# Optimization experiments

Measured on AMD Instinct MI355X. Metric: run time of the kernel, lower is better.

Reference implementation:

```python
import jax, jax.numpy as jnp
import numpy as np

EPS = 1e-12  # matches torch F.normalize default eps

def setup_inputs() -> dict:
    key = jax.random.key(0)
    k1, k2 = jax.random.split(key)
    n, d = 8192, 1024
    x = jax.random.normal(k1, (n, d), dtype=jnp.float32)
    weight = jax.random.normal(k2, (d, d), dtype=jnp.float32) * (2.0 / d) ** 0.5
    return {"x": x, "weight": weight}

def reference(x, weight):
    # L2-normalize rows (torch F.normalize, dim=1): x / max(||x||_2, eps)
    nrm = jnp.sqrt(jnp.sum(x * x, axis=1, keepdims=True))
    norm = x / jnp.maximum(nrm, EPS)
    # adjacency: cosine-similarity Gram matrix [n, n] (materialized as in source)
    adj = norm @ norm.T
    ax = adj @ x          # [n, d]
    axw = ax @ weight     # [n, d]
    return axw
```

## Files before the change

### kernel.cpp

```cpp
#include <hip/hip_runtime.h>
#include <stdint.h>

typedef unsigned short u16;
typedef unsigned int u32;
typedef __attribute__((ext_vector_type(8))) short short8;
typedef __attribute__((ext_vector_type(4))) float floatx4;

__device__ __forceinline__ u16 f2b(float f) {
    u32 u = __builtin_bit_cast(u32, f);
    return (u16)((u + 0x7fffu + ((u >> 16) & 1u)) >> 16);
}

__device__ __forceinline__ void gld16(const void* g, void* l) {
    __builtin_amdgcn_global_load_lds(
        (const __attribute__((address_space(1))) u32*)g,
        (__attribute__((address_space(3))) u32*)l, 16, 0, 0);
}

__global__ __launch_bounds__(256) void fuse_prep(
    const float* __restrict__ x, u16* __restrict__ YT, u16* __restrict__ Yn) {
    __shared__ float tile[32][129];
    int r0 = blockIdx.x * 32;
    int t = threadIdx.x;
    int tg = t >> 5, tl = t & 31;
    float ss[4] = {0.f, 0.f, 0.f, 0.f};
    for (int c = 0; c < 8; c++) {
        #pragma unroll
        for (int i = 0; i < 4; i++) {
            int rr = i * 8 + tg;
            float4 v = *(const float4*)(x + (long)(r0 + rr) * 1024 + c * 128 + tl * 4);
            ss[i] += v.x * v.x + v.y * v.y + v.z * v.z + v.w * v.w;
        }
    }
    float rs_[4], sr_[4];
    #pragma unroll
    for (int i = 0; i < 4; i++) {
        #pragma unroll
        for (int m = 16; m > 0; m >>= 1) ss[i] += __shfl_xor(ss[i], m);
        float rcp = 1.0f / fmaxf(sqrtf(ss[i]), 1e-12f);
        rs_[i] = rcp;
        sr_[i] = sqrtf(rcp);
    }
    for (int c = 0; c < 8; c++) {
        __syncthreads();
        #pragma unroll
        for (int i = 0; i < 4; i++) {
            int rr = i * 8 + tg;
            float4 v = *(const float4*)(x + (long)(r0 + rr) * 1024 + c * 128 + tl * 4);
            ushort4 o;
            o.x = f2b(v.x * rs_[i]); o.y = f2b(v.y * rs_[i]);
            o.z = f2b(v.z * rs_[i]); o.w = f2b(v.w * rs_[i]);
            *(ushort4*)(Yn + (long)(r0 + rr) * 1024 + c * 128 + tl * 4) = o;
            tile[rr][tl * 4 + 0] = v.x * sr_[i];
            tile[rr][tl * 4 + 1] = v.y * sr_[i];
            tile[rr][tl * 4 + 2] = v.z * sr_[i];
            tile[rr][tl * 4 + 3] = v.w * sr_[i];
        }
        __syncthreads();
        #pragma unroll
        for (int i = 0; i < 4; i++) {
            int lin = i * 256 + t;
            int cc = lin >> 3, r4 = (lin & 7) << 2;
            ushort4 o;
            o.x = f2b(tile[r4 + 0][cc]); o.y = f2b(tile[r4 + 1][cc]);
            o.z = f2b(tile[r4 + 2][cc]); o.w = f2b(tile[r4 + 3][cc]);
            *(ushort4*)(YT + (long)(c * 128 + cc) * 8192 + r0 + r4) = o;
        }
    }
}

__global__ __launch_bounds__(256) void transpose_scale_dual(
    const float* __restrict__ src, const float* __restrict__ sr,
    u16* __restrict__ dstT, u16* __restrict__ dstR, int rows, int cols) {
    __shared__ float tile[64][65];
    __shared__ float rbuf[64];
    int r0 = blockIdx.x * 64, c0 = blockIdx.y * 64;
    int t = threadIdx.x;
    if (t < 64) rbuf[t] = (sr != nullptr) ? sr[r0 + t] : 1.0f;
    __syncthreads();
    #pragma unroll
    for (int i = 0; i < 4; i++) {
        int lin = i * 256 + t;
        int rr = lin >> 4, c4 = (lin & 15) << 2;
        float4 v = *(const float4*)(src + (long)(r0 + rr) * cols + c0 + c4);
        float s = rbuf[rr];
        v.x *= s; v.y *= s; v.z *= s; v.w *= s;
        tile[rr][c4] = v.x; tile[rr][c4 + 1] = v.y; tile[rr][c4 + 2] = v.z; tile[rr][c4 + 3] = v.w;
        if (dstR != nullptr) {
            ushort4 o; o.x = f2b(v.x); o.y = f2b(v.y); o.z = f2b(v.z); o.w = f2b(v.w);
            *(ushort4*)(dstR + (long)(r0 + rr) * cols + c0 + c4) = o;
        }
    }
    __syncthreads();
    #pragma unroll
    for (int i = 0; i < 4; i++) {
        int lin = i * 256 + t;
        int cc = lin >> 4, r4 = (lin & 15) << 2;
        ushort4 o;
        o.x = f2b(tile[r4][cc]);
        o.y = f2b(tile[r4 + 1][cc]);
        o.z = f2b(tile[r4 + 2][cc]);
        o.w = f2b(tile[r4 + 3][cc]);
        *(ushort4*)(dstT + (long)(c0 + cc) * rows + r0 + r4) = o;
    }
}

__global__ __launch_bounds__(256) void reduce_sym64(
    const float* __restrict__ P, u16* __restrict__ D, int S, long E) {
    __shared__ float lt[64][65];
    int ti = blockIdx.x >> 4, tj = blockIdx.x & 15;
    int t = threadIdx.x;
    int r = t >> 4, c4 = (t & 15) << 2;
    int kept = (ti <= 2 * (tj >> 1) + 1);
    if (kept) {
        #pragma unroll
        for (int it = 0; it < 4; it++) {
            int row = 64 * ti + it * 16 + r;
            long idx = (long)row * 1024 + 64 * tj + c4;
            float4 s = *(const float4*)(P + idx);
            for (int z = 1; z < S; z++) {
                float4 v = *(const float4*)(P + (long)z * E + idx);
                s.x += v.x; s.y += v.y; s.z += v.z; s.w += v.w;
            }
            ushort4 o; o.x = f2b(s.x); o.y = f2b(s.y); o.z = f2b(s.z); o.w = f2b(s.w);
            *(ushort4*)(D + idx) = o;
        }
    } else {
        #pragma unroll
        for (int it = 0; it < 4; it++) {
            int row = it * 16 + r;
            long idx = (long)(64 * tj + row) * 1024 + 64 * ti + c4;
            float4 s = *(const float4*)(P + idx);
            for (int z = 1; z < S; z++) {
                float4 v = *(const float4*)(P + (long)z * E + idx);
                s.x += v.x; s.y += v.y; s.z += v.z; s.w += v.w;
            }
            lt[row][c4] = s.x; lt[row][c4 + 1] = s.y; lt[row][c4 + 2] = s.z; lt[row][c4 + 3] = s.w;
        }
        __syncthreads();
        #pragma unroll
        for (int it = 0; it < 4; it++) {
            int dr = it * 16 + r;
            ushort4 o;
            o.x = f2b(lt[c4 + 0][dr]); o.y = f2b(lt[c4 + 1][dr]);
            o.z = f2b(lt[c4 + 2][dr]); o.w = f2b(lt[c4 + 3][dr]);
            *(ushort4*)(D + (long)(64 * ti + dr) * 1024 + 64 * tj + c4) = o;
        }
    }
}

__global__ __launch_bounds__(256, 4) void gemm64x128(
    const u16* __restrict__ A, const u16* __restrict__ B,
    float* __restrict__ C, const float* __restrict__ rowscale,
    int lda, int ldb, int ldc, int tilesN, int kIters, long coffz, int sym, int obf16) {
    __shared__ __align__(16) u16 As[64 * 64];
    __shared__ __align__(16) u16 Bs[128 * 64];
    int bid = blockIdx.x;
    int nx = gridDim.x;
    if ((nx & 7) == 0) { int cpx = nx >> 3; bid = (bid & 7) * cpx + (bid >> 3); }
    int tm, tn;
    if (sym) {
        int id = bid, j = 0;
        while (true) {
            int c = (2 * j + 2 < 16) ? (2 * j + 2) : 16;
            if (id < c) break;
            id -= c; j++;
        }
        tn = j; tm = id;
    } else {
        tm = bid / tilesN; tn = bid % tilesN;
    }
    long kOff = (long)blockIdx.y * kIters * 64;
    const u16* Ap = A + (long)tm * 64 * lda + kOff;
    const u16* Bp = B + (long)tn * 128 * ldb + kOff;
    long coff = (long)blockIdx.y * coffz;

    int t = threadIdx.x;
    int lane = t & 63, w = t >> 6;
    int wm = (w & 1) * 32, wn = (w >> 1) * 64;
    int r16 = lane & 15, q = lane >> 4;

    int acl[2], bcl[4];
    #pragma unroll
    for (int j = 0; j < 2; j++) acl[j] = (w * 2 + j) * 64 + lane;
    #pragma unroll
    for (int j = 0; j < 4; j++) bcl[j] = (w * 4 + j) * 64 + lane;

    floatx4 acc[2][4];
    #pragma unroll
    for (int i = 0; i < 2; i++)
        #pragma unroll
        for (int j = 0; j < 4; j++) acc[i][j] = (floatx4){0.f, 0.f, 0.f, 0.f};

    for (int kt = 0; kt < kIters; kt++) {
        long kk = (long)kt * 64;
        #pragma unroll
        for (int j = 0; j < 2; j++) {
            int cl = acl[j], row = cl >> 3, cg = (cl & 7) ^ (row & 7);
            gld16(Ap + (long)row * lda + kk + cg * 8, (void*)&As[cl * 8]);
        }
        #pragma unroll
        for (int j = 0; j < 4; j++) {
            int cl = bcl[j], row = cl >> 3, cg = (cl & 7) ^ (row & 7);
            gld16(Bp + (long)row * ldb + kk + cg * 8, (void*)&Bs[cl * 8]);
        }
        __syncthreads();
        #pragma unroll
        for (int ks = 0; ks < 2; ks++) {
            short8 a[2], b[4];
            #pragma unroll
            for (int i = 0; i < 2; i++) {
                int rr = wm + i * 16 + r16;
                int cc = (ks * 4 + q) ^ (rr & 7);
                a[i] = *(const short8*)&As[rr * 64 + cc * 8];
            }
            #pragma unroll
            for (int j = 0; j < 4; j++) {
                int rr = wn + j * 16 + r16;
                int cc = (ks * 4 + q) ^ (rr & 7);
                b[j] = *(const short8*)&Bs[rr * 64 + cc * 8];
            }
            #pragma unroll
            for (int i = 0; i < 2; i++)
                #pragma unroll
                for (int j = 0; j < 4; j++)
                    acc[i][j] = __builtin_amdgcn_mfma_f32_16x16x32_bf16(a[i], b[j], acc[i][j], 0, 0, 0);
        }
        __syncthreads();
    }

    int m0 = tm * 64 + wm, n0 = tn * 128 + wn;
    #pragma unroll
    for (int i = 0; i < 2; i++) {
        int mm = m0 + i * 16 + q * 4;
        float rs[4];
        #pragma unroll
        for (int r = 0; r < 4; r++) rs[r] = (rowscale != nullptr) ? rowscale[mm + r] : 1.0f;
        #pragma unroll
        for (int j = 0; j < 4; j++) {
            int nn = n0 + j * 16 + r16;
            #pragma unroll
            for (int r = 0; r < 4; r++) {
                float v = acc[i][j][r] * rs[r];
                if (obf16) ((u16*)C)[coff + (long)(mm + r) * ldc + nn] = f2b(v);
                else       C[coff + (long)(mm + r) * ldc + nn] = v;
            }
        }
    }
}

__global__ __launch_bounds__(256) void gemm128(
    const u16* __restrict__ A, const u16* __restrict__ B,
    float* __restrict__ C, const float* __restrict__ rowscale,
    int lda, int ldb, int ldc, int tilesN, int kIters) {
    __shared__ __align__(16) u16 As[128 * 64];
    __shared__ __align__(16) u16 Bs[128 * 64];
    int bid = blockIdx.x;
    int nx = gridDim.x;
    if ((nx & 7) == 0) { int cpx = nx >> 3; bid = (bid & 7) * cpx + (bid >> 3); }
    int tm = bid / tilesN, tn = bid % tilesN;
    const u16* Ap = A + (long)tm * 128 * lda;
    const u16* Bp = B + (long)tn * 128 * ldb;

    int t = threadIdx.x;
    int lane = t & 63, w = t >> 6;
    int wm = (w & 1) * 64, wn = (w >> 1) * 64;
    int r16 = lane & 15, q = lane >> 4;

    floatx4 acc[4][4];
    #pragma unroll
    for (int i = 0; i < 4; i++)
        #pragma unroll
        for (int j = 0; j < 4; j++) acc[i][j] = (floatx4){0.f, 0.f, 0.f, 0.f};

    for (int kt = 0; kt < kIters; kt++) {
        long kk = (long)kt * 64;
        #pragma unroll
        for (int j = 0; j < 4; j++) {
            int cl = j * 256 + t, row = cl >> 3, cg = (cl & 7) ^ (row & 7);
            gld16(Ap + (long)row * lda + kk + cg * 8, (void*)&As[cl * 8]);
        }
        #pragma unroll
        for (int j = 0; j < 4; j++) {
            int cl = j * 256 + t, row = cl >> 3, cg = (cl & 7) ^ (row & 7);
            gld16(Bp + (long)row * ldb + kk + cg * 8, (void*)&Bs[cl * 8]);
        }
        __syncthreads();
        #pragma unroll
        for (int ks = 0; ks < 2; ks++) {
            short8 a[4], b[4];
            #pragma unroll
            for (int i = 0; i < 4; i++) {
                int rr = wm + i * 16 + r16;
                int cc = (ks * 4 + q) ^ (rr & 7);
                a[i] = *(const short8*)&As[rr * 64 + cc * 8];
            }
            #pragma unroll
            for (int j = 0; j < 4; j++) {
                int rr = wn + j * 16 + r16;
                int cc = (ks * 4 + q) ^ (rr & 7);
                b[j] = *(const short8*)&Bs[rr * 64 + cc * 8];
            }
            #pragma unroll
            for (int i = 0; i < 4; i++)
                #pragma unroll
                for (int j = 0; j < 4; j++)
                    acc[i][j] = __builtin_amdgcn_mfma_f32_16x16x32_bf16(a[i], b[j], acc[i][j], 0, 0, 0);
        }
        __syncthreads();
    }

    int m0 = tm * 128 + wm, n0 = tn * 128 + wn;
    #pragma unroll
    for (int i = 0; i < 4; i++) {
        int mm = m0 + i * 16 + q * 4;
        float rs[4];
        #pragma unroll
        for (int r = 0; r < 4; r++) rs[r] = (rowscale != nullptr) ? rowscale[mm + r] : 1.0f;
        #pragma unroll
        for (int j = 0; j < 4; j++) {
            int nn = n0 + j * 16 + r16;
            #pragma unroll
            for (int r = 0; r < 4; r++)
                C[(long)(mm + r) * ldc + nn] = acc[i][j][r] * rs[r];
        }
    }
}

extern "C" void kernel_launch(void* const* d_in, const int* in_sizes, int n_in,
                              void* d_out, int out_size, void* d_ws, size_t ws_size,
                              hipStream_t stream) {
    const float* x = (const float*)d_in[0];
    const float* wgt = (const float*)d_in[1];
    float* out = (float*)d_out;
    char* ws = (char*)d_ws;

    const size_t MB = 1048576;
    u16*   YT = (u16*)ws;
    u16*   Yn = (u16*)(ws + 16 * MB);
    u16*   Wt = (u16*)(ws + 32 * MB);
    u16*   Gb = (u16*)(ws + 34 * MB);
    u16*   Mt = (u16*)(ws + 36 * MB);
    float* Gp = (float*)(ws + 38 * MB);

    fuse_prep<<<256, 256, 0, stream>>>(x, YT, Yn);
    transpose_scale_dual<<<dim3(16, 16), 256, 0, stream>>>(wgt, nullptr, Wt, nullptr, 1024, 1024);
    gemm64x128<<<dim3(72, 8), 256, 0, stream>>>(YT, YT, Gp, nullptr,
                                                8192, 8192, 1024, 8, 16, 1048576, 1, 0);
    reduce_sym64<<<256, 256, 0, stream>>>(Gp, Gb, 8, 1048576);
    gemm64x128<<<dim3(128, 1), 256, 0, stream>>>(Wt, Gb, (float*)Mt, nullptr,
                                                 1024, 1024, 1024, 8, 16, 0, 0, 1);
    gemm128<<<dim3(512, 1), 256, 0, stream>>>(Yn, Mt, out, nullptr,
                                              1024, 1024, 1024, 8, 16);
}
```

Before: 170.6 us.

## Double GEMM K-tile to 128, merge prep kernels, halve symmetric reduce reads

All GEMMs now stage K tiles of 128 instead of 64 in LDS, with a 16-way XOR swizzle and half as many K iterations. This means half as many barriers per output tile, but LDS use per block goes up and occupancy drops (launch bounds lowered to 3 and 2). The x-normalize/transpose prep and the weight transpose are merged into one launch. The symmetric reduce now reads each kept tile once and writes both it and its mirror, so mirror blocks exit early instead of re-reading the partial sums.

```diff
diff --git a/kernel.cpp b/kernel.cpp
--- a/kernel.cpp
+++ b/kernel.cpp
@@ -17,126 +17,112 @@
         (__attribute__((address_space(3))) u32*)l, 16, 0, 0);
 }
 
-__global__ __launch_bounds__(256) void fuse_prep(
-    const float* __restrict__ x, u16* __restrict__ YT, u16* __restrict__ Yn) {
-    __shared__ float tile[32][129];
-    int r0 = blockIdx.x * 32;
+__global__ __launch_bounds__(256) void prep_all(
+    const float* __restrict__ x, const float* __restrict__ wgt,
+    u16* __restrict__ YT, u16* __restrict__ Yn, u16* __restrict__ Wt) {
+    __shared__ __align__(16) float sh[64 * 66];
+    int b = blockIdx.x;
     int t = threadIdx.x;
-    int tg = t >> 5, tl = t & 31;
-    float ss[4] = {0.f, 0.f, 0.f, 0.f};
-    for (int c = 0; c < 8; c++) {
+    if (b < 256) {
+        float (*tile)[129] = (float(*)[129])sh;
+        int r0 = b * 32;
+        int tg = t >> 5, tl = t & 31;
+        float ss[4] = {0.f, 0.f, 0.f, 0.f};
+        for (int c = 0; c < 8; c++) {
+            #pragma unroll
+            for (int i = 0; i < 4; i++) {
+                int rr = i * 8 + tg;
+                float4 v = *(const float4*)(x + (long)(r0 + rr) * 1024 + c * 128 + tl * 4);
+                ss[i] += v.x * v.x + v.y * v.y + v.z * v.z + v.w * v.w;
+            }
+        }
+        float rs_[4], sr_[4];
         #pragma unroll
         for (int i = 0; i < 4; i++) {
-            int rr = i * 8 + tg;
-            float4 v = *(const float4*)(x + (long)(r0 + rr) * 1024 + c * 128 + tl * 4);
-            ss[i] += v.x * v.x + v.y * v.y + v.z * v.z + v.w * v.w;
-        }
-    }
-    float rs_[4], sr_[4];
-    #pragma unroll
-    for (int i = 0; i < 4; i++) {
-        #pragma unroll
-        for (int m = 16; m > 0; m >>= 1) ss[i] += __shfl_xor(ss[i], m);
-        float rcp = 1.0f / fmaxf(sqrtf(ss[i]), 1e-12f);
-        rs_[i] = rcp;
-        sr_[i] = sqrtf(rcp);
-    }
-    for (int c = 0; c < 8; c++) {
-        __syncthreads();
-        #pragma unroll
-        for (int i = 0; i < 4; i++) {
-            int rr = i * 8 + tg;
-            float4 v = *(const float4*)(x + (long)(r0 + rr) * 1024 + c * 128 + tl * 4);
-            ushort4 o;
-            o.x = f2b(v.x * rs_[i]); o.y = f2b(v.y * rs_[i]);
-            o.z = f2b(v.z * rs_[i]); o.w = f2b(v.w * rs_[i]);
-            *(ushort4*)(Yn + (long)(r0 + rr) * 1024 + c * 128 + tl * 4) = o;
-            tile[rr][tl * 4 + 0] = v.x * sr_[i];
-            tile[rr][tl * 4 + 1] = v.y * sr_[i];
-            tile[rr][tl * 4 + 2] = v.z * sr_[i];
-            tile[rr][tl * 4 + 3] = v.w * sr_[i];
-        }
-        __syncthreads();
+            #pragma unroll
+            for (int m = 16; m > 0; m >>= 1) ss[i] += __shfl_xor(ss[i], m);
+            float rcp = 1.0f / fmaxf(sqrtf(ss[i]), 1e-12f);
+            rs_[i] = rcp;
+            sr_[i] = sqrtf(rcp);
+        }
+        for (int c = 0; c < 8; c++) {
+            __syncthreads();
+            #pragma unroll
+            for (int i = 0; i < 4; i++) {
+                int rr = i * 8 + tg;
+                float4 v = *(const float4*)(x + (long)(r0 + rr) * 1024 + c * 128 + tl * 4);
+                ushort4 o;
+                o.x = f2b(v.x * rs_[i]); o.y = f2b(v.y * rs_[i]);
+                o.z = f2b(v.z * rs_[i]); o.w = f2b(v.w * rs_[i]);
+                *(ushort4*)(Yn + (long)(r0 + rr) * 1024 + c * 128 + tl * 4) = o;
+                tile[rr][tl * 4 + 0] = v.x * sr_[i];
+                tile[rr][tl * 4 + 1] = v.y * sr_[i];
+                tile[rr][tl * 4 + 2] = v.z * sr_[i];
+                tile[rr][tl * 4 + 3] = v.w * sr_[i];
+            }
+            __syncthreads();
+            #pragma unroll
+            for (int i = 0; i < 4; i++) {
+                int lin = i * 256 + t;
+                int cc = lin >> 3, r4 = (lin & 7) << 2;
+                ushort4 o;
+                o.x = f2b(tile[r4 + 0][cc]); o.y = f2b(tile[r4 + 1][cc]);
+                o.z = f2b(tile[r4 + 2][cc]); o.w = f2b(tile[r4 + 3][cc]);
+                *(ushort4*)(YT + (long)(c * 128 + cc) * 8192 + r0 + r4) = o;
+            }
+        }
+    } else {
+        float (*tile)[65] = (float(*)[65])sh;
+        int bb = b - 256;
+        int r0 = (bb >> 4) * 64, c0 = (bb & 15) * 64;
         #pragma unroll
         for (int i = 0; i < 4; i++) {
             int lin = i * 256 + t;
-            int cc = lin >> 3, r4 = (lin & 7) << 2;
+            int rr = lin >> 4, c4 = (lin & 15) << 2;
+            float4 v = *(const float4*)(wgt + (long)(r0 + rr) * 1024 + c0 + c4);
+            tile[rr][c4] = v.x; tile[rr][c4 + 1] = v.y;
+            tile[rr][c4 + 2] = v.z; tile[rr][c4 + 3] = v.w;
+        }
+        __syncthreads();
+        #pragma unroll
+        for (int i = 0; i < 4; i++) {
+            int lin = i * 256 + t;
+            int cc = lin >> 4, r4 = (lin & 15) << 2;
             ushort4 o;
-            o.x = f2b(tile[r4 + 0][cc]); o.y = f2b(tile[r4 + 1][cc]);
-            o.z = f2b(tile[r4 + 2][cc]); o.w = f2b(tile[r4 + 3][cc]);
-            *(ushort4*)(YT + (long)(c * 128 + cc) * 8192 + r0 + r4) = o;
-        }
-    }
-}
-
-__global__ __launch_bounds__(256) void transpose_scale_dual(
-    const float* __restrict__ src, const float* __restrict__ sr,
-    u16* __restrict__ dstT, u16* __restrict__ dstR, int rows, int cols) {
-    __shared__ float tile[64][65];
-    __shared__ float rbuf[64];
-    int r0 = blockIdx.x * 64, c0 = blockIdx.y * 64;
-    int t = threadIdx.x;
-    if (t < 64) rbuf[t] = (sr != nullptr) ? sr[r0 + t] : 1.0f;
-    __syncthreads();
-    #pragma unroll
-    for (int i = 0; i < 4; i++) {
-        int lin = i * 256 + t;
-        int rr = lin >> 4, c4 = (lin & 15) << 2;
-        float4 v = *(const float4*)(src + (long)(r0 + rr) * cols + c0 + c4);
-        float s = rbuf[rr];
-        v.x *= s; v.y *= s; v.z *= s; v.w *= s;
-        tile[rr][c4] = v.x; tile[rr][c4 + 1] = v.y; tile[rr][c4 + 2] = v.z; tile[rr][c4 + 3] = v.w;
-        if (dstR != nullptr) {
-            ushort4 o; o.x = f2b(v.x); o.y = f2b(v.y); o.z = f2b(v.z); o.w = f2b(v.w);
-            *(ushort4*)(dstR + (long)(r0 + rr) * cols + c0 + c4) = o;
-        }
-    }
-    __syncthreads();
-    #pragma unroll
-    for (int i = 0; i < 4; i++) {
-        int lin = i * 256 + t;
-        int cc = lin >> 4, r4 = (lin & 15) << 2;
-        ushort4 o;
-        o.x = f2b(tile[r4][cc]);
-        o.y = f2b(tile[r4 + 1][cc]);
-        o.z = f2b(tile[r4 + 2][cc]);
-        o.w = f2b(tile[r4 + 3][cc]);
-        *(ushort4*)(dstT + (long)(c0 + cc) * rows + r0 + r4) = o;
-    }
-}
-
-__global__ __launch_bounds__(256) void reduce_sym64(
+            o.x = f2b(tile[r4][cc]);
+            o.y = f2b(tile[r4 + 1][cc]);
+            o.z = f2b(tile[r4 + 2][cc]);
+            o.w = f2b(tile[r4 + 3][cc]);
+            *(ushort4*)(Wt + (long)(c0 + cc) * 1024 + r0 + r4) = o;
+        }
+    }
+}
+
+__global__ __launch_bounds__(256) void reduce_symC(
     const float* __restrict__ P, u16* __restrict__ D, int S, long E) {
     __shared__ float lt[64][65];
     int ti = blockIdx.x >> 4, tj = blockIdx.x & 15;
+    if (ti > 2 * (tj >> 1) + 1) return;
+    int mir = (tj > 2 * (ti >> 1) + 1);
     int t = threadIdx.x;
     int r = t >> 4, c4 = (t & 15) << 2;
-    int kept = (ti <= 2 * (tj >> 1) + 1);
-    if (kept) {
-        #pragma unroll
-        for (int it = 0; it < 4; it++) {
-            int row = 64 * ti + it * 16 + r;
-            long idx = (long)row * 1024 + 64 * tj + c4;
-            float4 s = *(const float4*)(P + idx);
-            for (int z = 1; z < S; z++) {
-                float4 v = *(const float4*)(P + (long)z * E + idx);
-                s.x += v.x; s.y += v.y; s.z += v.z; s.w += v.w;
-            }
-            ushort4 o; o.x = f2b(s.x); o.y = f2b(s.y); o.z = f2b(s.z); o.w = f2b(s.w);
-            *(ushort4*)(D + idx) = o;
-        }
-    } else {
-        #pragma unroll
-        for (int it = 0; it < 4; it++) {
-            int row = it * 16 + r;
-            long idx = (long)(64 * tj + row) * 1024 + 64 * ti + c4;
-            float4 s = *(const float4*)(P + idx);
-            for (int z = 1; z < S; z++) {
-                float4 v = *(const float4*)(P + (long)z * E + idx);
-                s.x += v.x; s.y += v.y; s.z += v.z; s.w += v.w;
-            }
-            lt[row][c4] = s.x; lt[row][c4 + 1] = s.y; lt[row][c4 + 2] = s.z; lt[row][c4 + 3] = s.w;
-        }
+    #pragma unroll
+    for (int it = 0; it < 4; it++) {
+        int row = it * 16 + r;
+        long idx = (long)(64 * ti + row) * 1024 + 64 * tj + c4;
+        float4 s = *(const float4*)(P + idx);
+        for (int z = 1; z < S; z++) {
+            float4 v = *(const float4*)(P + (long)z * E + idx);
+            s.x += v.x; s.y += v.y; s.z += v.z; s.w += v.w;
+        }
+        ushort4 o; o.x = f2b(s.x); o.y = f2b(s.y); o.z = f2b(s.z); o.w = f2b(s.w);
+        *(ushort4*)(D + idx) = o;
+        if (mir) {
+            lt[row][c4] = s.x; lt[row][c4 + 1] = s.y;
+            lt[row][c4 + 2] = s.z; lt[row][c4 + 3] = s.w;
+        }
+    }
+    if (mir) {
         __syncthreads();
         #pragma unroll
         for (int it = 0; it < 4; it++) {
@@ -144,17 +130,17 @@
             ushort4 o;
             o.x = f2b(lt[c4 + 0][dr]); o.y = f2b(lt[c4 + 1][dr]);
             o.z = f2b(lt[c4 + 2][dr]); o.w = f2b(lt[c4 + 3][dr]);
-            *(ushort4*)(D + (long)(64 * ti + dr) * 1024 + 64 * tj + c4) = o;
-        }
-    }
-}
-
-__global__ __launch_bounds__(256, 4) void gemm64x128(
+            *(ushort4*)(D + (long)(64 * tj + dr) * 1024 + 64 * ti + c4) = o;
+        }
+    }
+}
+
+__global__ __launch_bounds__(256, 3) void gemm64x128(
     const u16* __restrict__ A, const u16* __restrict__ B,
     float* __restrict__ C, const float* __restrict__ rowscale,
     int lda, int ldb, int ldc, int tilesN, int kIters, long coffz, int sym, int obf16) {
-    __shared__ __align__(16) u16 As[64 * 64];
-    __shared__ __align__(16) u16 Bs[128 * 64];
+    __shared__ __align__(16) u16 As[64 * 128];
+    __shared__ __align__(16) u16 Bs[128 * 128];
     int bid = blockIdx.x;
     int nx = gridDim.x;
     if ((nx & 7) == 0) { int cpx = nx >> 3; bid = (bid & 7) * cpx + (bid >> 3); }
@@ -170,7 +156,7 @@
     } else {
         tm = bid / tilesN; tn = bid % tilesN;
     }
-    long kOff = (long)blockIdx.y * kIters * 64;
+    long kOff = (long)blockIdx.y * kIters * 128;
     const u16* Ap = A + (long)tm * 64 * lda + kOff;
     const u16* Bp = B + (long)tn * 128 * ldb + kOff;
     long coff = (long)blockIdx.y * coffz;
@@ -180,12 +166,6 @@
     int wm = (w & 1) * 32, wn = (w >> 1) * 64;
     int r16 = lane & 15, q = lane >> 4;
 
-    int acl[2], bcl[4];
-    #pragma unroll
-    for (int j = 0; j < 2; j++) acl[j] = (w * 2 + j) * 64 + lane;
-    #pragma unroll
-    for (int j = 0; j < 4; j++) bcl[j] = (w * 4 + j) * 64 + lane;
-
     floatx4 acc[2][4];
     #pragma unroll
     for (int i = 0; i < 2; i++)
@@ -193,32 +173,32 @@
         for (int j = 0; j < 4; j++) acc[i][j] = (floatx4){0.f, 0.f, 0.f, 0.f};
 
     for (int kt = 0; kt < kIters; kt++) {
-        long kk = (long)kt * 64;
-        #pragma unroll
-        for (int j = 0; j < 2; j++) {
-            int cl = acl[j], row = cl >> 3, cg = (cl & 7) ^ (row & 7);
+        long kk = (long)kt * 128;
+        #pragma unroll
+        for (int j = 0; j < 4; j++) {
+            int cl = j * 256 + t, row = cl >> 4, cg = (cl & 15) ^ (row & 15);
             gld16(Ap + (long)row * lda + kk + cg * 8, (void*)&As[cl * 8]);
         }
         #pragma unroll
-        for (int j = 0; j < 4; j++) {
-            int cl = bcl[j], row = cl >> 3, cg = (cl & 7) ^ (row & 7);
+        for (int j = 0; j < 8; j++) {
+            int cl = j * 256 + t, row = cl >> 4, cg = (cl & 15) ^ (row & 15);
             gld16(Bp + (long)row * ldb + kk + cg * 8, (void*)&Bs[cl * 8]);
         }
         __syncthreads();
         #pragma unroll
-        for (int ks = 0; ks < 2; ks++) {
+        for (int ks = 0; ks < 4; ks++) {
             short8 a[2], b[4];
             #pragma unroll
             for (int i = 0; i < 2; i++) {
                 int rr = wm + i * 16 + r16;
-                int cc = (ks * 4 + q) ^ (rr & 7);
-                a[i] = *(const short8*)&As[rr * 64 + cc * 8];
+                int cc = (ks * 4 + q) ^ (rr & 15);
+                a[i] = *(const short8*)&As[rr * 128 + cc * 8];
             }
             #pragma unroll
             for (int j = 0; j < 4; j++) {
                 int rr = wn + j * 16 + r16;
-                int cc = (ks * 4 + q) ^ (rr & 7);
-                b[j] = *(const short8*)&Bs[rr * 64 + cc * 8];
+                int cc = (ks * 4 + q) ^ (rr & 15);
+                b[j] = *(const short8*)&Bs[rr * 128 + cc * 8];
             }
             #pragma unroll
             for (int i = 0; i < 2; i++)
@@ -249,12 +229,12 @@
     }
 }
 
-__global__ __launch_bounds__(256) void gemm128(
+__global__ __launch_bounds__(256, 2) void gemm128(
     const u16* __restrict__ A, const u16* __restrict__ B,
     float* __restrict__ C, const float* __restrict__ rowscale,
     int lda, int ldb, int ldc, int tilesN, int kIters) {
-    __shared__ __align__(16) u16 As[128 * 64];
-    __shared__ __align__(16) u16 Bs[128 * 64];
+    __shared__ __align__(16) u16 As[128 * 128];
+    __shared__ __align__(16) u16 Bs[128 * 128];
     int bid = blockIdx.x;
     int nx = gridDim.x;
     if ((nx & 7) == 0) { int cpx = nx >> 3; bid = (bid & 7) * cpx + (bid >> 3); }
@@ -274,32 +254,32 @@
         for (int j = 0; j < 4; j++) acc[i][j] = (floatx4){0.f, 0.f, 0.f, 0.f};
 
     for (int kt = 0; kt < kIters; kt++) {
-        long kk = (long)kt * 64;
-        #pragma unroll
-        for (int j = 0; j < 4; j++) {
-            int cl = j * 256 + t, row = cl >> 3, cg = (cl & 7) ^ (row & 7);
+        long kk = (long)kt * 128;
+        #pragma unroll
+        for (int j = 0; j < 8; j++) {
+            int cl = j * 256 + t, row = cl >> 4, cg = (cl & 15) ^ (row & 15);
             gld16(Ap + (long)row * lda + kk + cg * 8, (void*)&As[cl * 8]);
         }
         #pragma unroll
-        for (int j = 0; j < 4; j++) {
-            int cl = j * 256 + t, row = cl >> 3, cg = (cl & 7) ^ (row & 7);
+        for (int j = 0; j < 8; j++) {
+            int cl = j * 256 + t, row = cl >> 4, cg = (cl & 15) ^ (row & 15);
             gld16(Bp + (long)row * ldb + kk + cg * 8, (void*)&Bs[cl * 8]);
         }
         __syncthreads();
         #pragma unroll
-        for (int ks = 0; ks < 2; ks++) {
+        for (int ks = 0; ks < 4; ks++) {
             short8 a[4], b[4];
             #pragma unroll
             for (int i = 0; i < 4; i++) {
                 int rr = wm + i * 16 + r16;
-                int cc = (ks * 4 + q) ^ (rr & 7);
-                a[i] = *(const short8*)&As[rr * 64 + cc * 8];
+                int cc = (ks * 4 + q) ^ (rr & 15);
+                a[i] = *(const short8*)&As[rr * 128 + cc * 8];
             }
             #pragma unroll
             for (int j = 0; j < 4; j++) {
                 int rr = wn + j * 16 + r16;
-                int cc = (ks * 4 + q) ^ (rr & 7);
-                b[j] = *(const short8*)&Bs[rr * 64 + cc * 8];
+                int cc = (ks * 4 + q) ^ (rr & 15);
+                b[j] = *(const short8*)&Bs[rr * 128 + cc * 8];
             }
             #pragma unroll
             for (int i = 0; i < 4; i++)
@@ -343,13 +323,12 @@
     u16*   Mt = (u16*)(ws + 36 * MB);
     float* Gp = (float*)(ws + 38 * MB);
 
-    fuse_prep<<<256, 256, 0, stream>>>(x, YT, Yn);
-    transpose_scale_dual<<<dim3(16, 16), 256, 0, stream>>>(wgt, nullptr, Wt, nullptr, 1024, 1024);
+    prep_all<<<512, 256, 0, stream>>>(x, wgt, YT, Yn, Wt);
     gemm64x128<<<dim3(72, 8), 256, 0, stream>>>(YT, YT, Gp, nullptr,
-                                                8192, 8192, 1024, 8, 16, 1048576, 1, 0);
-    reduce_sym64<<<256, 256, 0, stream>>>(Gp, Gb, 8, 1048576);
+                                                8192, 8192, 1024, 8, 8, 1048576, 1, 0);
+    reduce_symC<<<256, 256, 0, stream>>>(Gp, Gb, 8, 1048576);
     gemm64x128<<<dim3(128, 1), 256, 0, stream>>>(Wt, Gb, (float*)Mt, nullptr,
-                                                 1024, 1024, 1024, 8, 16, 0, 0, 1);
+                                                 1024, 1024, 1024, 8, 8, 0, 0, 1);
     gemm128<<<dim3(512, 1), 256, 0, stream>>>(Yn, Mt, out, nullptr,
-                                              1024, 1024, 1024, 8, 16);
-}
+                                              1024, 1024, 1024, 8, 8);
+}
```

Measured after the change: 162.3 us. -4.9%, faster.
